# Kernel optimization log

Hardware: AMD Instinct MI355X
Metric: run time of the kernel (lower is better)

The kernel has to match this reference:

```python
import jax, jax.numpy as jnp
import numpy as np

N, E, DIN, DH, H = 100000, 500000, 776, 128, 4
C = DH // H          # per-head channels = 32
NEG_SLOPE = 0.2      # PyG GATConv default
LN_EPS = 1e-5        # torch LayerNorm default


def layer_norm(x, g, b):
    mu = x.mean(-1, keepdims=True)
    var = ((x - mu) ** 2).mean(-1, keepdims=True)
    return (x - mu) / jnp.sqrt(var + LN_EPS) * g + b


def gat_conv(x, src, dst, W, att_src, att_dst, bias):
    """PyG GATConv(DH, DH//H, heads=H) with default add_self_loops=True."""
    loops = jnp.arange(N, dtype=src.dtype)
    s = jnp.concatenate([src, loops])  # [E+N]
    d = jnp.concatenate([dst, loops])
    h = (x @ W).reshape(N, H, C)                      # [N,H,C]
    a_s = (h * att_src).sum(-1)                       # [N,H]
    a_d = (h * att_dst).sum(-1)                       # [N,H]
    e = jax.nn.leaky_relu(a_s[s] + a_d[d], NEG_SLOPE)  # [E+N,H]
    m = jax.ops.segment_max(e, d, num_segments=N)     # per-dst max (stable softmax)
    ex = jnp.exp(e - m[d])
    z = jax.ops.segment_sum(ex, d, num_segments=N)
    alpha = ex / z[d]                                 # segment softmax over incoming edges
    out = jax.ops.segment_sum(h[s] * alpha[..., None], d, num_segments=N)  # [N,H,C]
    return out.reshape(N, H * C) + bias


def tgat_layer(x, src, dst, p):
    x_t = layer_norm(x, p['ln_a_g'], p['ln_a_b'])        # TemporalAttention == LayerNorm only
    x_g = gat_conv(x_t, src, dst, p['gat_W'], p['gat_as'], p['gat_ad'], p['gat_b'])
    return layer_norm(x_t + x_g, p['ln_b_g'], p['ln_b_b'])  # dropout is identity (eval)


def setup_inputs() -> dict:
    key = jax.random.key(0)
    ks = jax.random.split(key, 32)
    x = jax.random.normal(ks[0], (N, DIN), dtype=jnp.float32)
    edge_index = jax.random.randint(ks[1], (2, E), 0, N, dtype=jnp.int64)
    timestamps = jax.random.uniform(ks[2], (E,), dtype=jnp.float32)
    sc = 0.05
    d = {
        'x': x, 'edge_index': edge_index, 'timestamps': timestamps,
        'Wp': jax.random.normal(ks[3], (DIN, DH)) * sc,
        'bp': jnp.zeros((DH,)),
        'dp_W1': jax.random.normal(ks[4], (2 * DH, DH)) * sc,
        'dp_b1': jnp.zeros((DH,)),
        'dp_W2': jax.random.normal(ks[5], (DH, 1)) * sc,
        'dp_b2': jnp.zeros((1,)),
    }
    for i in (1, 2):
        k = jax.random.split(ks[5 + i], 4)
        d[f'l{i}_ln_a_g'] = jnp.ones((DH,)); d[f'l{i}_ln_a_b'] = jnp.zeros((DH,))
        d[f'l{i}_gat_W'] = jax.random.normal(k[0], (DH, DH)) * sc
        d[f'l{i}_gat_as'] = jax.random.normal(k[1], (H, C)) * 0.1
        d[f'l{i}_gat_ad'] = jax.random.normal(k[2], (H, C)) * 0.1
        d[f'l{i}_gat_b'] = jnp.zeros((DH,))
        d[f'l{i}_ln_b_g'] = jnp.ones((DH,)); d[f'l{i}_ln_b_b'] = jnp.zeros((DH,))
    return d


def reference(x, edge_index, timestamps, Wp, bp, dp_W1, dp_b1, dp_W2, dp_b2,
              l1_ln_a_g, l1_ln_a_b, l1_gat_W, l1_gat_as, l1_gat_ad, l1_gat_b, l1_ln_b_g, l1_ln_b_b,
              l2_ln_a_g, l2_ln_a_b, l2_gat_W, l2_gat_as, l2_gat_ad, l2_gat_b, l2_ln_b_g, l2_ln_b_b):
    src, dst = edge_index[0], edge_index[1]
    h = x @ Wp + bp  # input projection
    h = tgat_layer(h, src, dst, dict(ln_a_g=l1_ln_a_g, ln_a_b=l1_ln_a_b, gat_W=l1_gat_W,
                                     gat_as=l1_gat_as, gat_ad=l1_gat_ad, gat_b=l1_gat_b,
                                     ln_b_g=l1_ln_b_g, ln_b_b=l1_ln_b_b))
    h = tgat_layer(h, src, dst, dict(ln_a_g=l2_ln_a_g, ln_a_b=l2_ln_a_b, gat_W=l2_gat_W,
                                     gat_as=l2_gat_as, gat_ad=l2_gat_ad, gat_b=l2_gat_b,
                                     ln_b_g=l2_ln_b_g, ln_b_b=l2_ln_b_b))
    # task == 'diffusion': gather src/dst embeddings, cat, 2-layer MLP head -> [E,1]
    ef = jnp.concatenate([h[src], h[dst]], axis=-1)       # [E, 2*DH]
    hid = jax.nn.relu(ef @ dp_W1 + dp_b1)                 # dropout identity (eval)
    return hid @ dp_W2 + dp_b2
```

## Files before the change

### kernel.cpp

```cpp
#include <hip/hip_runtime.h>
#include <math.h>

#define NNODES 100000
#define NEDGES 500000
#define DIN 776
#define DH 128
#define NHEAD 4
#define NEG_SLOPE 0.2f
#define LN_EPS 1e-5f
#define KPAD 832
#define NT_PROJ 13

typedef __attribute__((ext_vector_type(8))) short short8v;
typedef __attribute__((ext_vector_type(4))) float f32x4;

__device__ inline unsigned int f2bf_u(float f) {
    unsigned int u = __float_as_uint(f);
    return (u + 0x7fffu + ((u >> 16) & 1u)) >> 16;
}
__device__ inline float bf2f_lo(unsigned int u) { return __uint_as_float(u << 16); }
__device__ inline float bf2f_hi(unsigned int u) { return __uint_as_float(u & 0xffff0000u); }

#define GLDS16(g, l)                                                      \
    __builtin_amdgcn_global_load_lds(                                     \
        (const __attribute__((address_space(1))) unsigned int*)(g),       \
        (__attribute__((address_space(3))) unsigned int*)(l), 16, 0, 0)

__global__ __launch_bounds__(256) void setup_kernel(const float* __restrict__ Wp,
                                                    const float* __restrict__ gW1,
                                                    const float* __restrict__ gW2,
                                                    const float* __restrict__ W1,
                                                    unsigned short* __restrict__ BtP,
                                                    unsigned short* __restrict__ BtG1,
                                                    unsigned short* __restrict__ BtG2,
                                                    unsigned short* __restrict__ Bt1a,
                                                    unsigned short* __restrict__ Bt1b,
                                                    int* __restrict__ cnt) {
    const int S0 = 128 * KPAD, S = 128 * 128;
    int idx = blockIdx.x * 256 + threadIdx.x;
    if (idx < S0) {
        const int n = idx / KPAD, k = idx % KPAD;
        BtP[idx] = (k < DIN) ? (unsigned short)f2bf_u(Wp[(size_t)k * 128 + n]) : (unsigned short)0;
        return;
    }
    idx -= S0;
    if (idx < S) {
        BtG1[idx] = (unsigned short)f2bf_u(gW1[(size_t)(idx & 127) * 128 + (idx >> 7)]);
        return;
    }
    idx -= S;
    if (idx < S) {
        BtG2[idx] = (unsigned short)f2bf_u(gW2[(size_t)(idx & 127) * 128 + (idx >> 7)]);
        return;
    }
    idx -= S;
    if (idx < S) {
        Bt1a[idx] = (unsigned short)f2bf_u(W1[(size_t)(idx & 127) * 128 + (idx >> 7)]);
        return;
    }
    idx -= S;
    if (idx < S) {
        Bt1b[idx] = (unsigned short)f2bf_u(W1[(size_t)(128 + (idx & 127)) * 128 + (idx >> 7)]);
        return;
    }
    idx -= S;
    if (idx < NNODES) cnt[idx] = 0;
}

__global__ __launch_bounds__(256) void gemm_proj(const float* __restrict__ A,
                                                 const unsigned short* __restrict__ Bt,
                                                 const float* __restrict__ bias,
                                                 float* __restrict__ C, int nrows) {
    constexpr int LSA = 72;
    __shared__ unsigned short As[128 * LSA];
    const int tid = threadIdx.x;
    const int row0 = blockIdx.x * 128;
    const int lane = tid & 63;
    const int wid = tid >> 6;
    const int wr = (wid >> 1) * 64, wc = (wid & 1) * 64;
    const int lrow = lane & 15, hi = lane >> 4, lk = hi * 8;

    int srowv[8], schk[8];
    bool sok[8];
#pragma unroll
    for (int i = 0; i < 8; ++i) {
        const int cid = i * 256 + tid;
        srowv[i] = cid >> 4;
        schk[i] = cid & 15;
        sok[i] = (row0 + srowv[i]) < nrows;
    }

    float4 f[8];
    auto loadA = [&](int t) {
#pragma unroll
        for (int i = 0; i < 8; ++i) {
            const int k = t * 64 + schk[i] * 4;
            f[i] = (sok[i] && (k + 4 <= DIN))
                       ? *(const float4*)(A + (size_t)(row0 + srowv[i]) * DIN + k)
                       : make_float4(0.f, 0.f, 0.f, 0.f);
        }
    };
    auto writeA = [&]() {
#pragma unroll
        for (int i = 0; i < 8; ++i) {
            uint2 q;
            q.x = f2bf_u(f[i].x) | (f2bf_u(f[i].y) << 16);
            q.y = f2bf_u(f[i].z) | (f2bf_u(f[i].w) << 16);
            *(uint2*)&As[srowv[i] * LSA + schk[i] * 4] = q;
        }
    };

    f32x4 acc[4][4];
#pragma unroll
    for (int m = 0; m < 4; ++m)
#pragma unroll
        for (int n = 0; n < 4; ++n) acc[m][n] = (f32x4){0.f, 0.f, 0.f, 0.f};

    loadA(0);
    for (int t = 0; t < NT_PROJ; ++t) {
        writeA();
        __syncthreads();
        if (t + 1 < NT_PROJ) loadA(t + 1);
#pragma unroll
        for (int ks = 0; ks < 2; ++ks) {
            short8v a[4], b[4];
#pragma unroll
            for (int m = 0; m < 4; ++m)
                a[m] = *(const short8v*)&As[(wr + m * 16 + lrow) * LSA + ks * 32 + lk];
#pragma unroll
            for (int n = 0; n < 4; ++n) {
                const int col = wc + n * 16 + lrow;
                b[n] = *(const short8v*)&Bt[(size_t)col * KPAD + t * 64 + ks * 32 + lk];
            }
#pragma unroll
            for (int m = 0; m < 4; ++m)
#pragma unroll
                for (int n = 0; n < 4; ++n)
                    acc[m][n] = __builtin_amdgcn_mfma_f32_16x16x32_bf16(a[m], b[n], acc[m][n], 0, 0, 0);
        }
        __syncthreads();
    }

    float bv[4];
#pragma unroll
    for (int n = 0; n < 4; ++n) bv[n] = bias[wc + n * 16 + lrow];
#pragma unroll
    for (int m = 0; m < 4; ++m) {
        const int rbase = row0 + wr + m * 16 + hi * 4;
#pragma unroll
        for (int j = 0; j < 4; ++j) {
            const int r = rbase + j;
            if (r < nrows) {
#pragma unroll
                for (int n = 0; n < 4; ++n)
                    C[(size_t)r * 128 + wc + n * 16 + lrow] = acc[m][n][j] + bv[n];
            }
        }
    }
}

template<bool ASAD, bool BIAS>
__global__ __launch_bounds__(256) void gemm_k128(const unsigned short* __restrict__ Ab,
                                                 const unsigned short* __restrict__ Bt,
                                                 const float* __restrict__ bias,
                                                 const float* __restrict__ gas,
                                                 const float* __restrict__ gad,
                                                 unsigned short* __restrict__ Cb,
                                                 float* __restrict__ a_s,
                                                 float* __restrict__ a_d, int nrows) {
    __shared__ unsigned short As[128 * 128];
    const int tid = threadIdx.x, lane = tid & 63, wid = tid >> 6;
    const int row0 = blockIdx.x * 128;
    const int lrow = lane & 15, hi = lane >> 4, lk = hi * 8;
    const int wr = (wid >> 1) * 64, wc = (wid & 1) * 64;

    {
        const int l4 = lane >> 4, le = lane & 15;
#pragma unroll
        for (int i = 0; i < 8; ++i) {
            const int row = wid * 32 + i * 4 + l4;
            const int kk = (le ^ ((i * 4 + l4) & 7)) << 3;
            const unsigned short* g = Ab + (size_t)(row0 + row) * 128 + kk;
            GLDS16(g, &As[wid * 4096 + i * 512]);
        }
    }
    __syncthreads();

    f32x4 acc[4][4];
#pragma unroll
    for (int m = 0; m < 4; ++m)
#pragma unroll
        for (int n = 0; n < 4; ++n) acc[m][n] = (f32x4){0.f, 0.f, 0.f, 0.f};

#pragma unroll
    for (int ks = 0; ks < 4; ++ks) {
        short8v a[4];
#pragma unroll
        for (int m = 0; m < 4; ++m) {
            const int row = wr + m * 16 + lrow;
            const int e = (ks * 32 + lk) ^ ((row & 7) << 3);
            a[m] = *(const short8v*)&As[row * 128 + e];
        }
#pragma unroll
        for (int n = 0; n < 4; ++n) {
            const int col = wc + n * 16 + lrow;
            const short8v b = *(const short8v*)&Bt[(size_t)col * 128 + ks * 32 + lk];
#pragma unroll
            for (int m = 0; m < 4; ++m)
                acc[m][n] = __builtin_amdgcn_mfma_f32_16x16x32_bf16(a[m], b, acc[m][n], 0, 0, 0);
        }
    }

#pragma unroll
    for (int m = 0; m < 4; ++m) {
        const int rbase = row0 + wr + m * 16 + hi * 4;
#pragma unroll
        for (int j = 0; j < 4; ++j) {
            const int r = rbase + j;
            if (r < nrows) {
#pragma unroll
                for (int n = 0; n < 4; ++n) {
                    const int col = wc + n * 16 + lrow;
                    const float bv = BIAS ? bias[col] : 0.f;
                    Cb[(size_t)r * 128 + col] = (unsigned short)f2bf_u(acc[m][n][j] + bv);
                }
            }
        }
    }

    if (ASAD) {
        const int h0 = (wid & 1) * 2;
        float vs[4], vd[4];
#pragma unroll
        for (int n = 0; n < 4; ++n) {
            const int ai = (h0 + (n >> 1)) * 32 + (n & 1) * 16 + lrow;
            vs[n] = gas[ai];
            vd[n] = gad[ai];
        }
#pragma unroll
        for (int m = 0; m < 4; ++m) {
#pragma unroll
            for (int j = 0; j < 4; ++j) {
                float ps0 = acc[m][0][j] * vs[0] + acc[m][1][j] * vs[1];
                float ps1 = acc[m][2][j] * vs[2] + acc[m][3][j] * vs[3];
                float pd0 = acc[m][0][j] * vd[0] + acc[m][1][j] * vd[1];
                float pd1 = acc[m][2][j] * vd[2] + acc[m][3][j] * vd[3];
#pragma unroll
                for (int o = 1; o < 16; o <<= 1) {
                    ps0 += __shfl_xor(ps0, o);
                    ps1 += __shfl_xor(ps1, o);
                    pd0 += __shfl_xor(pd0, o);
                    pd1 += __shfl_xor(pd1, o);
                }
                if (lrow == 0) {
                    const int r = row0 + wr + m * 16 + hi * 4 + j;
                    if (r < nrows) {
                        a_s[(size_t)r * 4 + h0] = ps0;
                        a_s[(size_t)r * 4 + h0 + 1] = ps1;
                        a_d[(size_t)r * 4 + h0] = pd0;
                        a_d[(size_t)r * 4 + h0 + 1] = pd1;
                    }
                }
            }
        }
    }
}

__global__ __launch_bounds__(256) void ln_kernel(const float* __restrict__ in,
                                                 const float* __restrict__ g,
                                                 const float* __restrict__ b,
                                                 float* __restrict__ out,
                                                 unsigned short* __restrict__ outb, int n) {
    const int wave = (blockIdx.x * blockDim.x + threadIdx.x) >> 6;
    const int lane = threadIdx.x & 63;
    if (wave >= n) return;
    const float2 v = reinterpret_cast<const float2*>(in + (size_t)wave * 128)[lane];
    float s = v.x + v.y;
    float sq = v.x * v.x + v.y * v.y;
#pragma unroll
    for (int o = 32; o; o >>= 1) { s += __shfl_xor(s, o); sq += __shfl_xor(sq, o); }
    const float mu = s * (1.f / 128.f);
    const float var = sq * (1.f / 128.f) - mu * mu;
    const float rinv = rsqrtf(var + LN_EPS);
    const float2 gg = reinterpret_cast<const float2*>(g)[lane];
    const float2 bb = reinterpret_cast<const float2*>(b)[lane];
    float2 o2;
    o2.x = (v.x - mu) * rinv * gg.x + bb.x;
    o2.y = (v.y - mu) * rinv * gg.y + bb.y;
    reinterpret_cast<float2*>(out + (size_t)wave * 128)[lane] = o2;
    reinterpret_cast<unsigned int*>(outb + (size_t)wave * 128)[lane] =
        f2bf_u(o2.x) | (f2bf_u(o2.y) << 16);
}

__global__ __launch_bounds__(256) void csr_hist(const int* __restrict__ dst,
                                                int* __restrict__ cnt, int ne, int n) {
    const int e = blockIdx.x * 256 + threadIdx.x;
    if (e >= ne + n) return;
    const int d = (e < ne) ? dst[e] : (e - ne);
    atomicAdd(&cnt[d], 1);
}

__global__ __launch_bounds__(256) void csr_scan1(const int* __restrict__ cnt,
                                                 int* __restrict__ offs,
                                                 int* __restrict__ bsum, int n) {
    __shared__ int lds[256];
    const int i = blockIdx.x * 256 + threadIdx.x;
    int v = (i < n) ? cnt[i] : 0;
    lds[threadIdx.x] = v;
    __syncthreads();
    int acc = v;
#pragma unroll
    for (int o = 1; o < 256; o <<= 1) {
        int t = (threadIdx.x >= o) ? lds[threadIdx.x - o] : 0;
        __syncthreads();
        acc += t;
        lds[threadIdx.x] = acc;
        __syncthreads();
    }
    if (i < n) offs[i] = acc - v;
    if (threadIdx.x == 255) bsum[blockIdx.x] = acc;
}

__global__ __launch_bounds__(512) void csr_scan2(int* __restrict__ bsum, int nb) {
    __shared__ int lds[512];
    const int t = threadIdx.x;
    int v = (t < nb) ? bsum[t] : 0;
    lds[t] = v;
    __syncthreads();
    int acc = v;
#pragma unroll
    for (int o = 1; o < 512; o <<= 1) {
        int x = (t >= o) ? lds[t - o] : 0;
        __syncthreads();
        acc += x;
        lds[t] = acc;
        __syncthreads();
    }
    if (t < nb) bsum[t] = acc - v;
}

__global__ __launch_bounds__(256) void csr_scan3(int* __restrict__ offs,
                                                 const int* __restrict__ bsum,
                                                 int* __restrict__ cur, int n, int total) {
    const int i = blockIdx.x * 256 + threadIdx.x;
    if (i < n) {
        const int o = offs[i] + bsum[blockIdx.x];
        offs[i] = o;
        cur[i] = o;
    }
    if (i == 0) offs[n] = total;
}

__global__ __launch_bounds__(256) void csr_scatter(const int* __restrict__ src,
                                                   const int* __restrict__ dst,
                                                   int* __restrict__ cur,
                                                   int* __restrict__ csr, int ne, int n) {
    const int e = blockIdx.x * 256 + threadIdx.x;
    if (e >= ne + n) return;
    int s, d;
    if (e < ne) { s = src[e]; d = dst[e]; } else { s = d = e - ne; }
    const int slot = atomicAdd(&cur[d], 1);
    csr[slot] = s;
}

template<int MODE>
__global__ __launch_bounds__(256) void aggr_ln_kernel(const int* __restrict__ csr,
                                                      const int* __restrict__ offs,
                                                      const float* __restrict__ a_s,
                                                      const float* __restrict__ a_d,
                                                      const unsigned short* __restrict__ hWb,
                                                      float* __restrict__ xt,
                                                      const float* __restrict__ gbias,
                                                      const float* __restrict__ g1,
                                                      const float* __restrict__ b1,
                                                      const float* __restrict__ g2,
                                                      const float* __restrict__ b2,
                                                      unsigned short* __restrict__ actb, int n) {
    const int d = (blockIdx.x * blockDim.x + threadIdx.x) >> 6;
    const int lane = threadIdx.x & 63;
    if (d >= n) return;
    const int h = lane >> 4;
    const int beg = offs[d], end = offs[d + 1];
    const float ad = a_d[(size_t)d * 4 + h];

    float z = 0.f, ax = 0.f, ay = 0.f;
    for (int c = beg; c < end; c += 64) {
        const int nj = min(64, end - c);
        const int idx = (c + lane < end) ? csr[c + lane] : 0;
        int j = 0;
        for (; j + 1 < nj; j += 2) {
            const int s0 = __shfl(idx, j);
            const int s1 = __shfl(idx, j + 1);
            const float as0 = a_s[(size_t)s0 * 4 + h];
            const float as1 = a_s[(size_t)s1 * 4 + h];
            const unsigned int u0 =
                reinterpret_cast<const unsigned int*>(hWb + (size_t)s0 * 128)[lane];
            const unsigned int u1 =
                reinterpret_cast<const unsigned int*>(hWb + (size_t)s1 * 128)[lane];
            float x0 = as0 + ad; x0 = x0 > 0.f ? x0 : NEG_SLOPE * x0;
            float x1 = as1 + ad; x1 = x1 > 0.f ? x1 : NEG_SLOPE * x1;
            const float p0 = __expf(x0);
            const float p1 = __expf(x1);
            z += p0 + p1;
            ax += p0 * bf2f_lo(u0) + p1 * bf2f_lo(u1);
            ay += p0 * bf2f_hi(u0) + p1 * bf2f_hi(u1);
        }
        if (j < nj) {
            const int s0 = __shfl(idx, j);
            float x0 = a_s[(size_t)s0 * 4 + h] + ad;
            x0 = x0 > 0.f ? x0 : NEG_SLOPE * x0;
            const float p0 = __expf(x0);
            const unsigned int u0 =
                reinterpret_cast<const unsigned int*>(hWb + (size_t)s0 * 128)[lane];
            z += p0;
            ax += p0 * bf2f_lo(u0);
            ay += p0 * bf2f_hi(u0);
        }
    }
    const float rz = 1.f / z;

    const float2 a = reinterpret_cast<const float2*>(xt + (size_t)d * 128)[lane];
    const float2 gb = reinterpret_cast<const float2*>(gbias)[lane];
    float2 v;
    v.x = a.x + ax * rz + gb.x;
    v.y = a.y + ay * rz + gb.y;
    float s = v.x + v.y, sq = v.x * v.x + v.y * v.y;
#pragma unroll
    for (int o = 32; o; o >>= 1) { s += __shfl_xor(s, o); sq += __shfl_xor(sq, o); }
    float mu = s * (1.f / 128.f);
    float rinv = rsqrtf(sq * (1.f / 128.f) - mu * mu + LN_EPS);
    const float2 gg1 = reinterpret_cast<const float2*>(g1)[lane];
    const float2 bb1 = reinterpret_cast<const float2*>(b1)[lane];
    float2 y;
    y.x = (v.x - mu) * rinv * gg1.x + bb1.x;
    y.y = (v.y - mu) * rinv * gg1.y + bb1.y;
    if (MODE == 0) {
        s = y.x + y.y; sq = y.x * y.x + y.y * y.y;
#pragma unroll
        for (int o = 32; o; o >>= 1) { s += __shfl_xor(s, o); sq += __shfl_xor(sq, o); }
        mu = s * (1.f / 128.f);
        rinv = rsqrtf(sq * (1.f / 128.f) - mu * mu + LN_EPS);
        const float2 gg2 = reinterpret_cast<const float2*>(g2)[lane];
        const float2 bb2 = reinterpret_cast<const float2*>(b2)[lane];
        float2 o2;
        o2.x = (y.x - mu) * rinv * gg2.x + bb2.x;
        o2.y = (y.y - mu) * rinv * gg2.y + bb2.y;
        reinterpret_cast<float2*>(xt + (size_t)d * 128)[lane] = o2;
        reinterpret_cast<unsigned int*>(actb + (size_t)d * 128)[lane] =
            f2bf_u(o2.x) | (f2bf_u(o2.y) << 16);
    } else {
        reinterpret_cast<unsigned int*>(actb + (size_t)d * 128)[lane] =
            f2bf_u(y.x) | (f2bf_u(y.y) << 16);
    }
}

__global__ __launch_bounds__(256) void head_kernel(const int* __restrict__ src,
                                                   const int* __restrict__ dst,
                                                   const unsigned short* __restrict__ Asb,
                                                   const unsigned short* __restrict__ Adb,
                                                   const float* __restrict__ W2,
                                                   const float* __restrict__ b2,
                                                   float* __restrict__ out, int ne) {
    const int wave = (blockIdx.x * blockDim.x + threadIdx.x) >> 6;
    const int lane = threadIdx.x & 63;
    const int e0 = wave * 64;
    if (e0 >= ne) return;
    const int nj = min(64, ne - e0);
    const bool valid = (e0 + lane) < ne;
    const int sidx = valid ? src[e0 + lane] : 0;
    const int didx = valid ? dst[e0 + lane] : 0;
    const float2 w = reinterpret_cast<const float2*>(W2)[lane];
    const float bb = b2[0];
    float outv = 0.f;
    for (int j = 0; j < nj; ++j) {
        const int s = __shfl(sidx, j);
        const int d = __shfl(didx, j);
        const unsigned int ua =
            reinterpret_cast<const unsigned int*>(Asb + (size_t)s * 128)[lane];
        const unsigned int ub =
            reinterpret_cast<const unsigned int*>(Adb + (size_t)d * 128)[lane];
        float h0 = bf2f_lo(ua) + bf2f_lo(ub); h0 = fmaxf(h0, 0.f);
        float h1 = bf2f_hi(ua) + bf2f_hi(ub); h1 = fmaxf(h1, 0.f);
        float t = h0 * w.x + h1 * w.y;
#pragma unroll
        for (int o = 32; o; o >>= 1) t += __shfl_xor(t, o);
        if (lane == j) outv = t + bb;
    }
    if (valid) out[e0 + lane] = outv;
}

extern "C" void kernel_launch(void* const* d_in, const int* in_sizes, int n_in,
                              void* d_out, int out_size, void* d_ws, size_t ws_size,
                              hipStream_t stream) {
    const int N = NNODES, E = NEDGES;
    const float* x  = (const float*)d_in[0];
    const int* ei   = (const int*)d_in[1];
    const int* src  = ei;
    const int* dst  = ei + E;
    const float* Wp = (const float*)d_in[3];
    const float* bp = (const float*)d_in[4];
    const float* W1 = (const float*)d_in[5];
    const float* b1 = (const float*)d_in[6];
    const float* W2 = (const float*)d_in[7];
    const float* b2 = (const float*)d_in[8];
    const float* l1_ln_a_g = (const float*)d_in[9];
    const float* l1_ln_a_b = (const float*)d_in[10];
    const float* gW1  = (const float*)d_in[11];
    const float* gas1 = (const float*)d_in[12];
    const float* gad1 = (const float*)d_in[13];
    const float* gb1  = (const float*)d_in[14];
    const float* l1_ln_b_g = (const float*)d_in[15];
    const float* l1_ln_b_b = (const float*)d_in[16];
    const float* l2_ln_a_g = (const float*)d_in[17];
    const float* l2_ln_a_b = (const float*)d_in[18];
    const float* gW2  = (const float*)d_in[19];
    const float* gas2 = (const float*)d_in[20];
    const float* gad2 = (const float*)d_in[21];
    const float* gb2  = (const float*)d_in[22];
    const float* l2_ln_b_g = (const float*)d_in[23];
    const float* l2_ln_b_b = (const float*)d_in[24];

    float* ws = (float*)d_ws;
    float* h    = ws;
    float* xt   = h + (size_t)N * 128;
    float* a_s  = xt + (size_t)N * 128;
    float* a_d  = a_s + (size_t)N * 4;
    unsigned short* actb = (unsigned short*)(a_d + (size_t)N * 4);
    unsigned short* hWb  = actb + (size_t)N * 128;
    unsigned short* Asb  = hWb + (size_t)N * 128;
    unsigned short* Adb  = Asb + (size_t)N * 128;
    unsigned short* BtP  = Adb + (size_t)N * 128;
    unsigned short* BtG1 = BtP + 128 * KPAD;
    unsigned short* BtG2 = BtG1 + 128 * 128;
    unsigned short* Bt1a = BtG2 + 128 * 128;
    unsigned short* Bt1b = Bt1a + 128 * 128;
    int* cnt  = (int*)(Bt1b + 128 * 128);
    int* offs = cnt + N;
    int* bsum = offs + N + 1;
    int* csr  = bsum + 512;

    const int gemmGrid = (N + 127) / 128;
    const int lnGrid = (N + 3) / 4;
    const int edgeTot = E + N;
    const int edgeGrid = (edgeTot + 255) / 256;
    const int scanBlocks = (N + 255) / 256;
    const int aggrGrid = (N * 64 + 255) / 256;
    const int headWaves = (E + 63) / 64;
    const int headGrid = (headWaves + 3) / 4;
    const int setupTot = 128 * KPAD + 4 * 128 * 128 + N;

    setup_kernel<<<(setupTot + 255) / 256, 256, 0, stream>>>(Wp, gW1, gW2, W1, BtP, BtG1,
                                                             BtG2, Bt1a, Bt1b, cnt);
    csr_hist<<<edgeGrid, 256, 0, stream>>>(dst, cnt, E, N);
    csr_scan1<<<scanBlocks, 256, 0, stream>>>(cnt, offs, bsum, N);
    csr_scan2<<<1, 512, 0, stream>>>(bsum, scanBlocks);
    csr_scan3<<<scanBlocks, 256, 0, stream>>>(offs, bsum, cnt, N, edgeTot);
    csr_scatter<<<edgeGrid, 256, 0, stream>>>(src, dst, cnt, csr, E, N);

    gemm_proj<<<gemmGrid, 256, 0, stream>>>(x, BtP, bp, h, N);
    ln_kernel<<<lnGrid, 256, 0, stream>>>(h, l1_ln_a_g, l1_ln_a_b, xt, actb, N);

    gemm_k128<true, false><<<gemmGrid, 256, 0, stream>>>(actb, BtG1, nullptr, gas1, gad1,
                                                         hWb, a_s, a_d, N);
    aggr_ln_kernel<0><<<aggrGrid, 256, 0, stream>>>(csr, offs, a_s, a_d, hWb, xt, gb1,
                                                    l1_ln_b_g, l1_ln_b_b, l2_ln_a_g,
                                                    l2_ln_a_b, actb, N);
    gemm_k128<true, false><<<gemmGrid, 256, 0, stream>>>(actb, BtG2, nullptr, gas2, gad2,
                                                         hWb, a_s, a_d, N);
    aggr_ln_kernel<1><<<aggrGrid, 256, 0, stream>>>(csr, offs, a_s, a_d, hWb, xt, gb2,
                                                    l2_ln_b_g, l2_ln_b_b, nullptr,
                                                    nullptr, actb, N);

    gemm_k128<false, true><<<gemmGrid, 256, 0, stream>>>(actb, Bt1a, b1, nullptr, nullptr,
                                                         Asb, nullptr, nullptr, N);
    gemm_k128<false, false><<<gemmGrid, 256, 0, stream>>>(actb, Bt1b, nullptr, nullptr,
                                                          nullptr, Adb, nullptr, nullptr, N);
    head_kernel<<<headGrid, 256, 0, stream>>>(src, dst, Asb, Adb, W2, b2,
                                              (float*)d_out, E);
}
```

Before: 468.2 us.

## Fuse input projection with LayerNorm and drop fp32 residual buffers

The input projection GEMM now applies bias and the first LayerNorm in its epilogue, reducing row statistics across waves through shared memory and writing only bf16 activations. The separate LN kernel and the fp32 h/xt buffers go away, and the aggregation kernel reads the residual from the bf16 activation buffer instead of fp32 xt. The edge loop in aggregation is unrolled from 2 to 4 for more memory-level parallelism. This cuts a full fp32 write and read of N×128 per layer at the cost of reading the residual in bf16, which loses some precision.

After: 480.2 us. 2.6% more time.

```diff
diff --git a/kernel.cpp b/kernel.cpp
--- a/kernel.cpp
+++ b/kernel.cpp
@@ -67,10 +67,13 @@
     if (idx < NNODES) cnt[idx] = 0;
 }
 
-__global__ __launch_bounds__(256) void gemm_proj(const float* __restrict__ A,
-                                                 const unsigned short* __restrict__ Bt,
-                                                 const float* __restrict__ bias,
-                                                 float* __restrict__ C, int nrows) {
+__global__ __launch_bounds__(256) void gemm_proj_ln(const float* __restrict__ A,
+                                                    const unsigned short* __restrict__ Bt,
+                                                    const float* __restrict__ bias,
+                                                    const float* __restrict__ lng,
+                                                    const float* __restrict__ lnb,
+                                                    unsigned short* __restrict__ actb,
+                                                    int nrows) {
     constexpr int LSA = 72;
     __shared__ unsigned short As[128 * LSA];
     const int tid = threadIdx.x;
@@ -141,25 +144,69 @@
         __syncthreads();
     }
 
-    float bv[4];
-#pragma unroll
-    for (int n = 0; n < 4; ++n) bv[n] = bias[wc + n * 16 + lrow];
+    float bv[4], gv[4], bb[4];
+#pragma unroll
+    for (int n = 0; n < 4; ++n) {
+        const int col = wc + n * 16 + lrow;
+        bv[n] = bias[col];
+        gv[n] = lng[col];
+        bb[n] = lnb[col];
+    }
+#pragma unroll
+    for (int m = 0; m < 4; ++m)
+#pragma unroll
+        for (int n = 0; n < 4; ++n)
+#pragma unroll
+            for (int j = 0; j < 4; ++j) acc[m][n][j] += bv[n];
+
+    float* part = (float*)As;
 #pragma unroll
     for (int m = 0; m < 4; ++m) {
-        const int rbase = row0 + wr + m * 16 + hi * 4;
 #pragma unroll
         for (int j = 0; j < 4; ++j) {
-            const int r = rbase + j;
-            if (r < nrows) {
-#pragma unroll
-                for (int n = 0; n < 4; ++n)
-                    C[(size_t)r * 128 + wc + n * 16 + lrow] = acc[m][n][j] + bv[n];
+            float s = 0.f, sq = 0.f;
+#pragma unroll
+            for (int n = 0; n < 4; ++n) {
+                const float a = acc[m][n][j];
+                s += a;
+                sq += a * a;
             }
-        }
-    }
-}
-
-template<bool ASAD, bool BIAS>
+#pragma unroll
+            for (int o = 1; o < 16; o <<= 1) {
+                s += __shfl_xor(s, o);
+                sq += __shfl_xor(sq, o);
+            }
+            if (lrow == 0) {
+                const int r = wr + m * 16 + hi * 4 + j;
+                part[r * 4 + (wid & 1) * 2] = s;
+                part[r * 4 + (wid & 1) * 2 + 1] = sq;
+            }
+        }
+    }
+    __syncthreads();
+#pragma unroll
+    for (int m = 0; m < 4; ++m) {
+#pragma unroll
+        for (int j = 0; j < 4; ++j) {
+            const int rloc = wr + m * 16 + hi * 4 + j;
+            const int rg = row0 + rloc;
+            const float4 p = *(const float4*)&part[rloc * 4];
+            const float s = p.x + p.z, sq = p.y + p.w;
+            const float mu = s * (1.f / 128.f);
+            const float rinv = rsqrtf(sq * (1.f / 128.f) - mu * mu + LN_EPS);
+            if (rg < nrows) {
+#pragma unroll
+                for (int n = 0; n < 4; ++n) {
+                    const int col = wc + n * 16 + lrow;
+                    const float o = (acc[m][n][j] - mu) * rinv * gv[n] + bb[n];
+                    actb[(size_t)rg * 128 + col] = (unsigned short)f2bf_u(o);
+                }
+            }
+        }
+    }
+}
+
+template<bool ASAD>
 __global__ __launch_bounds__(256) void gemm_k128(const unsigned short* __restrict__ Ab,
                                                  const unsigned short* __restrict__ Bt,
                                                  const float* __restrict__ bias,
@@ -211,6 +258,7 @@
         }
     }
 
+    const bool hasBias = (bias != nullptr);
 #pragma unroll
     for (int m = 0; m < 4; ++m) {
         const int rbase = row0 + wr + m * 16 + hi * 4;
@@ -221,7 +269,7 @@
 #pragma unroll
                 for (int n = 0; n < 4; ++n) {
                     const int col = wc + n * 16 + lrow;
-                    const float bv = BIAS ? bias[col] : 0.f;
+                    const float bv = hasBias ? bias[col] : 0.f;
                     Cb[(size_t)r * 128 + col] = (unsigned short)f2bf_u(acc[m][n][j] + bv);
                 }
             }
@@ -266,32 +314,6 @@
     }
 }
 
-__global__ __launch_bounds__(256) void ln_kernel(const float* __restrict__ in,
-                                                 const float* __restrict__ g,
-                                                 const float* __restrict__ b,
-                                                 float* __restrict__ out,
-                                                 unsigned short* __restrict__ outb, int n) {
-    const int wave = (blockIdx.x * blockDim.x + threadIdx.x) >> 6;
-    const int lane = threadIdx.x & 63;
-    if (wave >= n) return;
-    const float2 v = reinterpret_cast<const float2*>(in + (size_t)wave * 128)[lane];
-    float s = v.x + v.y;
-    float sq = v.x * v.x + v.y * v.y;
-#pragma unroll
-    for (int o = 32; o; o >>= 1) { s += __shfl_xor(s, o); sq += __shfl_xor(sq, o); }
-    const float mu = s * (1.f / 128.f);
-    const float var = sq * (1.f / 128.f) - mu * mu;
-    const float rinv = rsqrtf(var + LN_EPS);
-    const float2 gg = reinterpret_cast<const float2*>(g)[lane];
-    const float2 bb = reinterpret_cast<const float2*>(b)[lane];
-    float2 o2;
-    o2.x = (v.x - mu) * rinv * gg.x + bb.x;
-    o2.y = (v.y - mu) * rinv * gg.y + bb.y;
-    reinterpret_cast<float2*>(out + (size_t)wave * 128)[lane] = o2;
-    reinterpret_cast<unsigned int*>(outb + (size_t)wave * 128)[lane] =
-        f2bf_u(o2.x) | (f2bf_u(o2.y) << 16);
-}
-
 __global__ __launch_bounds__(256) void csr_hist(const int* __restrict__ dst,
                                                 int* __restrict__ cnt, int ne, int n) {
     const int e = blockIdx.x * 256 + threadIdx.x;
@@ -369,7 +391,6 @@
                                                       const float* __restrict__ a_s,
                                                       const float* __restrict__ a_d,
                                                       const unsigned short* __restrict__ hWb,
-                                                      float* __restrict__ xt,
                                                       const float* __restrict__ gbias,
                                                       const float* __restrict__ g1,
                                                       const float* __restrict__ b1,
@@ -388,30 +409,35 @@
         const int nj = min(64, end - c);
         const int idx = (c + lane < end) ? csr[c + lane] : 0;
         int j = 0;
-        for (; j + 1 < nj; j += 2) {
+        for (; j + 3 < nj; j += 4) {
             const int s0 = __shfl(idx, j);
             const int s1 = __shfl(idx, j + 1);
+            const int s2 = __shfl(idx, j + 2);
+            const int s3 = __shfl(idx, j + 3);
             const float as0 = a_s[(size_t)s0 * 4 + h];
             const float as1 = a_s[(size_t)s1 * 4 + h];
-            const unsigned int u0 =
-                reinterpret_cast<const unsigned int*>(hWb + (size_t)s0 * 128)[lane];
-            const unsigned int u1 =
-                reinterpret_cast<const unsigned int*>(hWb + (size_t)s1 * 128)[lane];
+            const float as2 = a_s[(size_t)s2 * 4 + h];
+            const float as3 = a_s[(size_t)s3 * 4 + h];
+            const unsigned int u0 = reinterpret_cast<const unsigned int*>(hWb + (size_t)s0 * 128)[lane];
+            const unsigned int u1 = reinterpret_cast<const unsigned int*>(hWb + (size_t)s1 * 128)[lane];
+            const unsigned int u2 = reinterpret_cast<const unsigned int*>(hWb + (size_t)s2 * 128)[lane];
+            const unsigned int u3 = reinterpret_cast<const unsigned int*>(hWb + (size_t)s3 * 128)[lane];
             float x0 = as0 + ad; x0 = x0 > 0.f ? x0 : NEG_SLOPE * x0;
             float x1 = as1 + ad; x1 = x1 > 0.f ? x1 : NEG_SLOPE * x1;
-            const float p0 = __expf(x0);
-            const float p1 = __expf(x1);
-            z += p0 + p1;
-            ax += p0 * bf2f_lo(u0) + p1 * bf2f_lo(u1);
-            ay += p0 * bf2f_hi(u0) + p1 * bf2f_hi(u1);
-        }
-        if (j < nj) {
+            float x2 = as2 + ad; x2 = x2 > 0.f ? x2 : NEG_SLOPE * x2;
+            float x3 = as3 + ad; x3 = x3 > 0.f ? x3 : NEG_SLOPE * x3;
+            const float p0 = __expf(x0), p1 = __expf(x1);
+            const float p2 = __expf(x2), p3 = __expf(x3);
+            z += (p0 + p1) + (p2 + p3);
+            ax += p0 * bf2f_lo(u0) + p1 * bf2f_lo(u1) + p2 * bf2f_lo(u2) + p3 * bf2f_lo(u3);
+            ay += p0 * bf2f_hi(u0) + p1 * bf2f_hi(u1) + p2 * bf2f_hi(u2) + p3 * bf2f_hi(u3);
+        }
+        for (; j < nj; ++j) {
             const int s0 = __shfl(idx, j);
             float x0 = a_s[(size_t)s0 * 4 + h] + ad;
             x0 = x0 > 0.f ? x0 : NEG_SLOPE * x0;
             const float p0 = __expf(x0);
-            const unsigned int u0 =
-                reinterpret_cast<const unsigned int*>(hWb + (size_t)s0 * 128)[lane];
+            const unsigned int u0 = reinterpret_cast<const unsigned int*>(hWb + (size_t)s0 * 128)[lane];
             z += p0;
             ax += p0 * bf2f_lo(u0);
             ay += p0 * bf2f_hi(u0);
@@ -419,11 +445,11 @@
     }
     const float rz = 1.f / z;
 
-    const float2 a = reinterpret_cast<const float2*>(xt + (size_t)d * 128)[lane];
+    const unsigned int tu = reinterpret_cast<const unsigned int*>(actb + (size_t)d * 128)[lane];
     const float2 gb = reinterpret_cast<const float2*>(gbias)[lane];
     float2 v;
-    v.x = a.x + ax * rz + gb.x;
-    v.y = a.y + ay * rz + gb.y;
+    v.x = bf2f_lo(tu) + ax * rz + gb.x;
+    v.y = bf2f_hi(tu) + ay * rz + gb.y;
     float s = v.x + v.y, sq = v.x * v.x + v.y * v.y;
 #pragma unroll
     for (int o = 32; o; o >>= 1) { s += __shfl_xor(s, o); sq += __shfl_xor(sq, o); }
@@ -445,7 +471,6 @@
         float2 o2;
         o2.x = (y.x - mu) * rinv * gg2.x + bb2.x;
         o2.y = (y.y - mu) * rinv * gg2.y + bb2.y;
-        reinterpret_cast<float2*>(xt + (size_t)d * 128)[lane] = o2;
         reinterpret_cast<unsigned int*>(actb + (size_t)d * 128)[lane] =
             f2bf_u(o2.x) | (f2bf_u(o2.y) << 16);
     } else {
@@ -521,9 +546,7 @@
     const float* l2_ln_b_b = (const float*)d_in[24];
 
     float* ws = (float*)d_ws;
-    float* h    = ws;
-    float* xt   = h + (size_t)N * 128;
-    float* a_s  = xt + (size_t)N * 128;
+    float* a_s  = ws;
     float* a_d  = a_s + (size_t)N * 4;
     unsigned short* actb = (unsigned short*)(a_d + (size_t)N * 4);
     unsigned short* hWb  = actb + (size_t)N * 128;
@@ -540,7 +563,6 @@
     int* csr  = bsum + 512;
 
     const int gemmGrid = (N + 127) / 128;
-    const int lnGrid = (N + 3) / 4;
     const int edgeTot = E + N;
     const int edgeGrid = (edgeTot + 255) / 256;
     const int scanBlocks = (N + 255) / 256;
@@ -557,24 +579,23 @@
     csr_scan3<<<scanBlocks, 256, 0, stream>>>(offs, bsum, cnt, N, edgeTot);
     csr_scatter<<<edgeGrid, 256, 0, stream>>>(src, dst, cnt, csr, E, N);
 
-    gemm_proj<<<gemmGrid, 256, 0, stream>>>(x, BtP, bp, h, N);
-    ln_kernel<<<lnGrid, 256, 0, stream>>>(h, l1_ln_a_g, l1_ln_a_b, xt, actb, N);
-
-    gemm_k128<true, false><<<gemmGrid, 256, 0, stream>>>(actb, BtG1, nullptr, gas1, gad1,
-                                                         hWb, a_s, a_d, N);
-    aggr_ln_kernel<0><<<aggrGrid, 256, 0, stream>>>(csr, offs, a_s, a_d, hWb, xt, gb1,
+    gemm_proj_ln<<<gemmGrid, 256, 0, stream>>>(x, BtP, bp, l1_ln_a_g, l1_ln_a_b, actb, N);
+
+    gemm_k128<true><<<gemmGrid, 256, 0, stream>>>(actb, BtG1, nullptr, gas1, gad1,
+                                                  hWb, a_s, a_d, N);
+    aggr_ln_kernel<0><<<aggrGrid, 256, 0, stream>>>(csr, offs, a_s, a_d, hWb, gb1,
                                                     l1_ln_b_g, l1_ln_b_b, l2_ln_a_g,
                                                     l2_ln_a_b, actb, N);
-    gemm_k128<true, false><<<gemmGrid, 256, 0, stream>>>(actb, BtG2, nullptr, gas2, gad2,
-                                                         hWb, a_s, a_d, N);
-    aggr_ln_kernel<1><<<aggrGrid, 256, 0, stream>>>(csr, offs, a_s, a_d, hWb, xt, gb2,
+    gemm_k128<true><<<gemmGrid, 256, 0, stream>>>(actb, BtG2, nullptr, gas2, gad2,
+                                                  hWb, a_s, a_d, N);
+    aggr_ln_kernel<1><<<aggrGrid, 256, 0, stream>>>(csr, offs, a_s, a_d, hWb, gb2,
                                                     l2_ln_b_g, l2_ln_b_b, nullptr,
                                                     nullptr, actb, N);
 
-    gemm_k128<false, true><<<gemmGrid, 256, 0, stream>>>(actb, Bt1a, b1, nullptr, nullptr,
-                                                         Asb, nullptr, nullptr, N);
-    gemm_k128<false, false><<<gemmGrid, 256, 0, stream>>>(actb, Bt1b, nullptr, nullptr,
-                                                          nullptr, Adb, nullptr, nullptr, N);
+    gemm_k128<false><<<gemmGrid, 256, 0, stream>>>(actb, Bt1a, b1, nullptr, nullptr,
+                                                   Asb, nullptr, nullptr, N);
+    gemm_k128<false><<<gemmGrid, 256, 0, stream>>>(actb, Bt1b, nullptr, nullptr, nullptr,
+                                                   Adb, nullptr, nullptr, N);
     head_kernel<<<headGrid, 256, 0, stream>>>(src, dst, Asb, Adb, W2, b2,
                                               (float*)d_out, E);
 }
```
